# Kernel optimization log

Hardware: AMD Instinct MI355X
Metric: run time of the kernel (lower is better)

The kernel has to match this reference:

```python
import jax, jax.numpy as jnp
import numpy as np

N = 50000   # nodes
E = 800000  # edges (avg degree 16)
F = 16      # input node feature dim
H = 64      # hidden_channels
G = 128     # number of graphs
L = 3       # num_layers
OUT = 8     # output_channels


def _glorot(key, shape):
    fan = shape[-2] + shape[-1]
    return jax.random.normal(key, shape, dtype=jnp.float32) * jnp.sqrt(2.0 / fan)


def setup_inputs() -> dict:
    key = jax.random.key(0)
    ks = jax.random.split(key, 16)
    z = lambda *s: jnp.zeros(s, jnp.float32)
    return {
        "x": jax.random.normal(ks[0], (N, F), jnp.float32),
        "pos": jax.random.normal(ks[1], (N, 3), jnp.float32),
        "edge_index": jax.random.randint(ks[2], (2, E), 0, N),
        "batch": jnp.sort(jax.random.randint(ks[3], (N,), 0, G)),
        "node_W1": _glorot(ks[4], (F, H)), "node_b1": z(H),
        "node_W2": _glorot(ks[5], (H, H)), "node_b2": z(H),
        "local_W1": _glorot(ks[6], (L, 2 * H + 3, H)), "local_b1": z(L, H),
        "local_W2": _glorot(ks[7], (L, H, H)), "local_b2": z(L, H),
        "global_W1": _glorot(ks[8], (L, H, H)), "global_b1": z(L, H),
        "global_W2": _glorot(ks[9], (L, H, H)), "global_b2": z(L, H),
        "lin1_W": _glorot(ks[10], (H, H // 2)), "lin1_b": z(H // 2),
        "lin2_W": _glorot(ks[11], (H // 2, OUT)), "lin2_b": z(OUT),
    }


def reference(x, pos, edge_index, batch,
              node_W1, node_b1, node_W2, node_b2,
              local_W1, local_b1, local_W2, local_b2,
              global_W1, global_b1, global_W2, global_b2,
              lin1_W, lin1_b, lin2_W, lin2_b):
    n = x.shape[0]
    src, dst = edge_index[0], edge_index[1]  # x_j = x[src], x_i = x[dst]
    # node_lin: Linear -> ReLU -> Linear
    h = jnp.maximum(x @ node_W1 + node_b1, 0.0) @ node_W2 + node_b2
    for l in range(L):
        # message: cat([x_i, x_j, pos_j]) -> local_nn (Linear, ReLU, Linear)
        m = jnp.concatenate([h[dst], h[src], pos[src]], axis=-1)  # [E, 2H+3]
        m = jnp.maximum(m @ local_W1[l] + local_b1[l], 0.0) @ local_W2[l] + local_b2[l]
        # aggregate: scatter-add over destination nodes
        agg = jax.ops.segment_sum(m, dst, num_segments=n)
        # global_nn (Linear, ReLU, Linear), then outer ReLU from forward loop
        h = jnp.maximum(agg @ global_W1[l] + global_b1[l], 0.0) @ global_W2[l] + global_b2[l]
        h = jnp.maximum(h, 0.0)
    h = jnp.maximum(h @ lin1_W + lin1_b, 0.0)
    out = h @ lin2_W + lin2_b  # [N, OUT]
    # graph readout: scatter-add over batch ids
    return jax.ops.segment_sum(out, batch, num_segments=G)  # [G, OUT]
```

## Files before the change

### kernel.cpp

```cpp
#include <hip/hip_runtime.h>

#define N_NODES 50000
#define N_EDGES 800000
#define NGRAPH  128
#define XPITCH  72
#define NB      391
#define HEPB    4096
#define SEPB    8192
#define HBLKS   ((N_EDGES + HEPB - 1) / HEPB)
#define NGRP    3125
#define STRIDE  64
#define SENT    N_NODES

typedef short bf16x8 __attribute__((ext_vector_type(8)));
typedef float f32x4  __attribute__((ext_vector_type(4)));


__device__ __forceinline__ float atomAddF(float* p, float v) {
#if defined(__gfx950__) || defined(__AMDGCN__)
    return unsafeAtomicAdd(p, v);
#else
    return atomicAdd(p, v);
#endif
}

__device__ __forceinline__ unsigned short f2bf(float x) {
    unsigned u = __builtin_bit_cast(unsigned, x);
    u += 0x7fffu + ((u >> 16) & 1u);
    return (unsigned short)(u >> 16);
}
__device__ __forceinline__ float bf2f(unsigned short h) {
    return __builtin_bit_cast(float, (unsigned)h << 16);
}

__device__ __forceinline__ f32x4 mk4(float b) { f32x4 a = {b, b, b, b}; return a; }

template<int NKC, int KROW>
__device__ __forceinline__ f32x4 w_tile(const bf16x8* a,
                                        const unsigned short* __restrict__ Wm,
                                        int nt, int col, int quad, f32x4 acc) {
    const unsigned short* wp = Wm + (nt * 16 + col) * KROW + quad * 8;
#pragma unroll
    for (int c = 0; c < NKC; ++c) {
        bf16x8 b = *(const bf16x8*)(wp + c * 32);
        acc = __builtin_amdgcn_mfma_f32_16x16x32_bf16(a[c], b, acc, 0, 0, 0);
    }
    return acc;
}

template<int NKC>
__device__ __forceinline__ void a_load(const unsigned short* __restrict__ sl,
                                       int col, int quad, bf16x8* a) {
    a[0] = *(const bf16x8*)(sl + col * XPITCH + quad * 8);
    if (NKC > 1) a[1] = *(const bf16x8*)(sl + col * XPITCH + quad * 8 + 32);
}

__device__ __forceinline__ void w_store1(unsigned short* __restrict__ sl,
                                         int wv, int col, int quad, f32x4 acc,
                                         bool relu) {
#pragma unroll
    for (int r = 0; r < 4; ++r) {
        float x = acc[r];
        if (relu) x = fmaxf(x, 0.f);
        sl[(quad * 4 + r) * XPITCH + wv * 16 + col] = f2bf(x);
    }
}

__device__ __forceinline__ void g_store1(unsigned short* __restrict__ g, int gn0,
                                         int wv, int col, int quad, f32x4 acc) {
#pragma unroll
    for (int r = 0; r < 4; ++r) {
        int node = gn0 + quad * 4 + r;
        if (node < N_NODES)
            g[(size_t)node * 64 + wv * 16 + col] = f2bf(acc[r]);
    }
}

__device__ __forceinline__ void wave_agg4(const int* dg, unsigned short* __restrict__ sl,
                                          const unsigned short* __restrict__ u,
                                          const unsigned short* __restrict__ vin,
                                          const unsigned short* __restrict__ srcList,
                                          int gn0, int wv, int lane) {
    int sub = lane & 15, q = lane >> 4;
    int n0 = gn0 + wv * 4;
    ushort4 uu4[4];
#pragma unroll
    for (int mi = 0; mi < 4; ++mi)
        uu4[mi] = *(const ushort4*)(u + (size_t)(n0 + mi) * 64 + sub * 4);

#pragma unroll
    for (int mi = 0; mi < 4; ++mi) {
        int m = wv * 4 + mi;
        float u0 = bf2f(uu4[mi].x), u1 = bf2f(uu4[mi].y);
        float u2 = bf2f(uu4[mi].z), u3 = bf2f(uu4[mi].w);
        int pdeg = (dg[m] + 15) & ~15;
        size_t b = (size_t)(n0 + mi) * STRIDE;
        float a0 = 0.f, a1 = 0.f, a2 = 0.f, a3 = 0.f;

        for (int g0 = 0; g0 < pdeg; g0 += 16) {
            ushort4 ss = *(const ushort4*)(srcList + b + g0 + 4 * q);
            int s0 = ss.x, s1 = ss.y, s2 = ss.z, s3 = ss.w;
            ushort4 w0 = *(const ushort4*)(vin + (size_t)s0 * 64 + sub * 4);
            ushort4 w1 = *(const ushort4*)(vin + (size_t)s1 * 64 + sub * 4);
            ushort4 w2 = *(const ushort4*)(vin + (size_t)s2 * 64 + sub * 4);
            ushort4 w3 = *(const ushort4*)(vin + (size_t)s3 * 64 + sub * 4);
            a0 += fmaxf(u0 + bf2f(w0.x), 0.f) + fmaxf(u0 + bf2f(w1.x), 0.f)
                + fmaxf(u0 + bf2f(w2.x), 0.f) + fmaxf(u0 + bf2f(w3.x), 0.f);
            a1 += fmaxf(u1 + bf2f(w0.y), 0.f) + fmaxf(u1 + bf2f(w1.y), 0.f)
                + fmaxf(u1 + bf2f(w2.y), 0.f) + fmaxf(u1 + bf2f(w3.y), 0.f);
            a2 += fmaxf(u2 + bf2f(w0.z), 0.f) + fmaxf(u2 + bf2f(w1.z), 0.f)
                + fmaxf(u2 + bf2f(w2.z), 0.f) + fmaxf(u2 + bf2f(w3.z), 0.f);
            a3 += fmaxf(u3 + bf2f(w0.w), 0.f) + fmaxf(u3 + bf2f(w1.w), 0.f)
                + fmaxf(u3 + bf2f(w2.w), 0.f) + fmaxf(u3 + bf2f(w3.w), 0.f);
        }

        a0 += __shfl_xor(a0, 16); a0 += __shfl_xor(a0, 32);
        a1 += __shfl_xor(a1, 16); a1 += __shfl_xor(a1, 32);
        a2 += __shfl_xor(a2, 16); a2 += __shfl_xor(a2, 32);
        a3 += __shfl_xor(a3, 16); a3 += __shfl_xor(a3, 32);

        if (q == 0) {
            ushort4 o;
            o.x = f2bf(a0); o.y = f2bf(a1); o.z = f2bf(a2); o.w = f2bf(a3);
            *(ushort4*)&sl[m * XPITCH + sub * 4] = o;
        }
    }
}

#define OFF_NW1T  0
#define OFF_NW2T  2048
#define OFF_LYR   6144
#define LYR_SZ    20480
#define OFF_LIN1T 67584
#define OFF_LIN2T 69632
#define WT_TOTAL  70144

__global__ __launch_bounds__(256) void kPrep(
    const float* __restrict__ nW1, const float* __restrict__ lW1,
    const float* __restrict__ gW2,
    const float* __restrict__ lin1W, const float* __restrict__ lin2W,
    unsigned short* __restrict__ WT, int* __restrict__ gHist,
    int* __restrict__ doneCnt, float* __restrict__ out,
    unsigned short* __restrict__ v0, unsigned short* __restrict__ v1) {
    int i = blockIdx.x * 256 + threadIdx.x;
    if (blockIdx.x == 0) {
        for (int k = threadIdx.x; k < NB; k += 256) gHist[k] = 0;
        for (int k = threadIdx.x; k < NGRAPH * 8; k += 256) out[k] = 0.f;
        if (threadIdx.x == 0) *doneCnt = 0;
    }
    if (i < 64) {
        v0[(size_t)N_NODES * 64 + i] = 0xFF80;
        v1[(size_t)N_NODES * 64 + i] = 0xFF80;
    }
    if (i >= WT_TOTAL) return;
    int j = i;
    if (j < 2048) {
        int n = j >> 5, k = j & 31;
        WT[i] = (k < 16) ? f2bf(nW1[k * 64 + n]) : 0;
        return;
    }
    j -= 2048;
    if (j < 4096) return;
    j -= 4096;
    if (j < 3 * LYR_SZ) {
        int l = j / LYR_SZ;  j -= l * LYR_SZ;
        int m = j >> 12;     j &= 4095;
        if (m == 2 || m == 3 || (l == 0 && m < 2)) return;
        int n = j >> 6, k = j & 63;
        const float* src;
        if (m == 0)      src = lW1 + (size_t)l * 131 * 64;
        else if (m == 1) src = lW1 + (size_t)l * 131 * 64 + 64 * 64;
        else             src = gW2 + (size_t)l * 4096;
        WT[i] = f2bf(src[k * 64 + n]);
        return;
    }
    j -= 3 * LYR_SZ;
    if (j < 2048) {
        int n = j >> 6, k = j & 63;
        WT[i] = f2bf(lin1W[k * 32 + n]);
        return;
    }
    j -= 2048;
    {
        int n = j >> 5, k = j & 31;
        WT[i] = (n < 8) ? f2bf(lin2W[k * 8 + n]) : 0;
    }
}

__global__ __launch_bounds__(256) void kHist(
    const int* __restrict__ ei, int* __restrict__ gHist,
    int* __restrict__ bucketOff, int* __restrict__ cursor,
    int* __restrict__ doneCnt,
    const float* __restrict__ nW2, const float* __restrict__ lW1,
    const float* __restrict__ lW2, const float* __restrict__ gW1,
    const float* __restrict__ nb2, const float* __restrict__ lb1,
    const float* __restrict__ lb2,
    unsigned short* __restrict__ WT, float* __restrict__ fb) {
    __shared__ int h[NB];
    __shared__ int s0[512], s1[512];
    __shared__ int amLast;
    __shared__ float foldP[64 * 65];
    int tid = threadIdx.x;

    if (blockIdx.x >= HBLKS) {
        int f = blockIdx.x - HBLKS;
        const float* Wl;
        const float* Wr;
        size_t slot;
        if (f == 0)      { Wl = nW2;          Wr = lW1;            slot = OFF_LYR; }
        else if (f == 1) { Wl = nW2;          Wr = lW1 + 64 * 64;  slot = OFF_LYR + 4096; }
        else { int l = f - 2;
               Wl = lW2 + (size_t)l * 4096;   Wr = gW1 + (size_t)l * 4096;
               slot = OFF_LYR + (size_t)l * LYR_SZ + 2 * 4096; }

        int n = tid & 63;
        int w = tid >> 6;
        float acc[16];
#pragma unroll
        for (int i2 = 0; i2 < 16; ++i2) acc[i2] = 0.f;
        for (int t0 = 0; t0 < 64; t0 += 16) {
            float wr[16];
#pragma unroll
            for (int tt = 0; tt < 16; ++tt) wr[tt] = Wr[(t0 + tt) * 64 + n];
#pragma unroll
            for (int i2 = 0; i2 < 16; ++i2) {
                int kk = w * 16 + i2;
#pragma unroll
                for (int tt = 0; tt < 16; ++tt)
                    acc[i2] += Wl[kk * 64 + t0 + tt] * wr[tt];
            }
        }
#pragma unroll
        for (int i2 = 0; i2 < 16; ++i2)
            foldP[(w * 16 + i2) * 65 + n] = acc[i2];
        __syncthreads();
        for (int idx = tid; idx < 4096; idx += 256) {
            int nn = idx >> 6, kk = idx & 63;
            WT[slot + idx] = f2bf(foldP[kk * 65 + nn]);
        }
        if (tid < 64) {
            if (f == 0) {
                float s = 0.f;
                for (int t = 0; t < 64; ++t) s += nb2[t] * lW1[t * 64 + tid];
                fb[tid] = s;
            } else if (f == 1) {
                float s = 0.f;
                for (int t = 0; t < 64; ++t) s += nb2[t] * lW1[(64 + t) * 64 + tid];
                fb[64 + tid] = s + lb1[tid];
            } else {
                int l = f - 2;
                float s = 0.f;
                for (int t = 0; t < 64; ++t)
                    s += lb2[l * 64 + t] * gW1[(size_t)l * 4096 + t * 64 + tid];
                fb[128 + l * 64 + tid] = s;
            }
        }
        return;
    }

    for (int i = tid; i < NB; i += 256) h[i] = 0;
    __syncthreads();
    int base = blockIdx.x * HEPB;
#pragma unroll
    for (int k = 0; k < HEPB; k += 256) {
        int e = base + k + tid;
        if (e < N_EDGES) atomicAdd(&h[ei[N_EDGES + e] >> 7], 1);
    }
    __syncthreads();
    for (int i = tid; i < NB; i += 256)
        if (h[i]) atomicAdd(&gHist[i], h[i]);

    __threadfence();
    if (tid == 0) amLast = (atomicAdd(doneCnt, 1) == HBLKS - 1);
    __syncthreads();
    if (!amLast) return;
    __threadfence();

    for (int e = tid; e < 512; e += 256)
        s0[e] = (e < NB) ? atomicAdd(&gHist[e], 0) : 0;
    __syncthreads();
    int* sp = s0; int* dp = s1;
    for (int off = 1; off < 512; off <<= 1) {
        for (int e = tid; e < 512; e += 256)
            dp[e] = sp[e] + ((e >= off) ? sp[e - off] : 0);
        __syncthreads();
        int* t = sp; sp = dp; dp = t;
    }
    for (int e = tid; e < NB; e += 256) {
        int cnt = atomicAdd(&gHist[e], 0);
        int excl = sp[e] - cnt;
        bucketOff[e] = excl;
        cursor[e] = excl;
    }
    if (tid == 0) bucketOff[NB] = sp[NB - 1];
}

__global__ __launch_bounds__(256) void kScat(const int* __restrict__ ei,
                                             int* __restrict__ cursor,
                                             int* __restrict__ packs) {
    __shared__ int sdata[SEPB];
    __shared__ int hist[NB];
    __shared__ int loff[NB + 1];
    __shared__ int gbase[NB];
    __shared__ int sc0[512], sc1[512];
    int tid = threadIdx.x;
    int base = blockIdx.x * SEPB;
    int nE = min(SEPB, N_EDGES - base);

    for (int i = tid; i < NB; i += 256) hist[i] = 0;
    __syncthreads();

    int myPack[SEPB / 256];
    unsigned short myRank[SEPB / 256];
#pragma unroll
    for (int kk = 0; kk < SEPB / 256; ++kk) {
        int e = base + kk * 256 + tid;
        if (e < N_EDGES) {
            int s = ei[e], d = ei[N_EDGES + e];
            myPack[kk] = (s << 16) | d;
            myRank[kk] = (unsigned short)atomicAdd(&hist[d >> 7], 1);
        }
    }
    __syncthreads();

    for (int e = tid; e < 512; e += 256) sc0[e] = (e < NB) ? hist[e] : 0;
    __syncthreads();
    int* sp = sc0; int* dp = sc1;
    for (int off = 1; off < 512; off <<= 1) {
        for (int e = tid; e < 512; e += 256)
            dp[e] = sp[e] + ((e >= off) ? sp[e - off] : 0);
        __syncthreads();
        int* t = sp; sp = dp; dp = t;
    }
    for (int e = tid; e < NB; e += 256) loff[e] = sp[e] - hist[e];
    if (tid == 0) loff[NB] = sp[NB - 1];
    __syncthreads();

    for (int e = tid; e < NB; e += 256)
        gbase[e] = hist[e] ? atomicAdd(&cursor[e], hist[e]) : 0;
#pragma unroll
    for (int kk = 0; kk < SEPB / 256; ++kk) {
        int e = base + kk * 256 + tid;
        if (e < N_EDGES) {
            int p = myPack[kk];
            int b = (p & 0xffff) >> 7;
            sdata[loff[b] + myRank[kk]] = p;
        }
    }
    __syncthreads();

    for (int i = tid; i < nE; i += 256) {
        int p = sdata[i];
        int b = (p & 0xffff) >> 7;
        packs[gbase[b] + (i - loff[b])] = p;
    }
}

__global__ __launch_bounds__(256) void kSortA(
    const int* __restrict__ bucketOff, const int* __restrict__ packs,
    unsigned short* __restrict__ srcList, int* __restrict__ degArr,
    const float* __restrict__ x, const float* __restrict__ pos,
    const unsigned short* __restrict__ WT, const float* __restrict__ fb,
    const float* __restrict__ nb1,
    const float* __restrict__ lW1f,
    unsigned short* __restrict__ u, unsigned short* __restrict__ v) {
    __shared__ int cur[128];
    __shared__ unsigned short SL[2][16 * XPITCH];
    __shared__ float pw[48];

    int tid = threadIdx.x;
    if (blockIdx.x < NB) {
        int nbk = blockIdx.x;
        int nodeBase = nbk * 128;
        int nvalid = min(128, N_NODES - nodeBase);
        int eb = bucketOff[nbk], ee = bucketOff[nbk + 1];

        if (tid < 128) cur[tid] = 0;
        __syncthreads();
        for (int i = eb + tid; i < ee; i += 256) {
            int p = packs[i];
            int node = p & 127;
            int r = atomicAdd(&cur[node], 1);
            if (r < STRIDE)
                srcList[(size_t)(nodeBase + node) * STRIDE + r] =
                    (unsigned short)(((unsigned)p) >> 16);
        }
        __syncthreads();
        if (tid < nvalid) {
            int d = min(cur[tid], STRIDE);
            degArr[nodeBase + tid] = d;
            int pd = (d + 15) & ~15;
            size_t b2 = (size_t)(nodeBase + tid) * STRIDE;
            for (int r = d; r < pd; ++r) srcList[b2 + r] = (unsigned short)SENT;
        }
        return;
    }

    int gn0 = (blockIdx.x - NB) * 16;
    int lane = tid & 63;
    int wv = __builtin_amdgcn_readfirstlane(tid >> 6);
    int col = lane & 15, quad = lane >> 4;

    for (int idx = tid; idx < 512; idx += 256) {
        int m = idx >> 5, k = idx & 31;
        int node = gn0 + m;
        float val = (k < 16) ? x[(size_t)node * 16 + k] : 0.f;
        SL[0][m * XPITCH + k] = f2bf(val);
    }
    if (tid < 48) {
        int node = gn0 + tid / 3;
        pw[tid] = pos[(size_t)node * 3 + tid % 3];
    }
    __syncthreads();

    bf16x8 a[2];
    f32x4 acc;

    a_load<1>(SL[0], col, quad, a);
    acc = w_tile<1, 32>(a, WT + OFF_NW1T, wv, col, quad, mk4(nb1[wv * 16 + col]));
    w_store1(SL[1], wv, col, quad, acc, true);
    __syncthreads();

    const unsigned short* FA = WT + OFF_LYR;
    const unsigned short* FB = FA + 4096;
    const float* W1c = lW1f + 128 * 64;
    int ch = wv * 16 + col;

    a_load<2>(SL[1], col, quad, a);
    acc = w_tile<2, 64>(a, FA, wv, col, quad, mk4(fb[ch]));
    g_store1(u, gn0, wv, col, quad, acc);

    acc = w_tile<2, 64>(a, FB, wv, col, quad, mk4(fb[64 + ch]));
    float w0 = W1c[ch], w1 = W1c[64 + ch], w2 = W1c[128 + ch];
#pragma unroll
    for (int r = 0; r < 4; ++r) {
        int rr = quad * 4 + r;
        acc[r] += pw[rr * 3 + 0] * w0 + pw[rr * 3 + 1] * w1 + pw[rr * 3 + 2] * w2;
    }
    g_store1(v, gn0, wv, col, quad, acc);
}

__global__ __launch_bounds__(256) void kB(
    const float* __restrict__ pos, const int* __restrict__ degArr,
    const unsigned short* __restrict__ srcList,
    const unsigned short* __restrict__ WT, const float* __restrict__ fb, int l,
    const float* __restrict__ gb1, const float* __restrict__ gb2,
    const float* __restrict__ lW1f_next, const float* __restrict__ b1n,
    unsigned short* __restrict__ u,
    const unsigned short* __restrict__ vin,
    unsigned short* __restrict__ vout) {
    __shared__ unsigned short SL[2][16 * XPITCH];
    __shared__ float pw[48];
    __shared__ int dgW[16];
    int tid = threadIdx.x;
    int lane = tid & 63;
    int wv = __builtin_amdgcn_readfirstlane(tid >> 6);
    int gn0 = blockIdx.x * 16;
    int col = lane & 15, quad = lane >> 4;

    const unsigned short* LYR = WT + OFF_LYR + (size_t)l * LYR_SZ;
    const unsigned short* GT   = LYR + 2 * 4096;
    const unsigned short* gW2T = LYR + 4 * 4096;
    const unsigned short* aTn = WT + OFF_LYR + (size_t)(l + 1) * LYR_SZ;
    const unsigned short* bTn = aTn + 4096;
    const float* lbg = fb + 128 + l * 64;

    if (tid < 48) {
        int node = gn0 + tid / 3;
        pw[tid] = pos[(size_t)node * 3 + tid % 3];
    }
    if (tid < 16) dgW[tid] = degArr[gn0 + tid];
    __syncthreads();

    wave_agg4(dgW, SL[0], u, vin, srcList, gn0, wv, lane);
    __syncthreads();

    bf16x8 a[2];
    f32x4 acc;
    float dgr[4];
#pragma unroll
    for (int r = 0; r < 4; ++r) dgr[r] = (float)dgW[quad * 4 + r];

    int ch = wv * 16 + col;
    {
        float bb = lbg[ch];
        float g1 = gb1[ch];
        f32x4 init = {dgr[0] * bb + g1, dgr[1] * bb + g1,
                      dgr[2] * bb + g1, dgr[3] * bb + g1};
        a_load<2>(SL[0], col, quad, a);
        acc = w_tile<2, 64>(a, GT, wv, col, quad, init);
    }
    w_store1(SL[1], wv, col, quad, acc, true);
    __syncthreads();

    a_load<2>(SL[1], col, quad, a);
    acc = w_tile<2, 64>(a, gW2T, wv, col, quad, mk4(gb2[ch]));
    w_store1(SL[0], wv, col, quad, acc, true);
    __syncthreads();

    a_load<2>(SL[0], col, quad, a);
    acc = w_tile<2, 64>(a, aTn, wv, col, quad, mk4(0.f));
    g_store1(u, gn0, wv, col, quad, acc);

    const float* W1c = lW1f_next + 128 * 64;
    acc = w_tile<2, 64>(a, bTn, wv, col, quad, mk4(b1n[ch]));
    float w0 = W1c[ch], w1 = W1c[64 + ch], w2 = W1c[128 + ch];
#pragma unroll
    for (int r = 0; r < 4; ++r) {
        int rr = quad * 4 + r;
        acc[r] += pw[rr * 3 + 0] * w0 + pw[rr * 3 + 1] * w1 + pw[rr * 3 + 2] * w2;
    }
    g_store1(vout, gn0, wv, col, quad, acc);
}

__global__ __launch_bounds__(256) void kC(
    const int* __restrict__ degArr, const unsigned short* __restrict__ srcList,
    const int* __restrict__ batch, const unsigned short* __restrict__ WT,
    const float* __restrict__ fb,
    const float* __restrict__ gb1, const float* __restrict__ gb2,
    const float* __restrict__ lin1b, const float* __restrict__ lin2b,
    const unsigned short* __restrict__ u, const unsigned short* __restrict__ vin,
    float* __restrict__ out) {
    __shared__ unsigned short SL[2][16 * XPITCH];
    __shared__ int dgW[16];
    __shared__ int batchW[16];
    __shared__ float bins[16 * 8];
    int tid = threadIdx.x;
    int lane = tid & 63;
    int wv = __builtin_amdgcn_readfirstlane(tid >> 6);
    int gn0 = blockIdx.x * 16;
    int col = lane & 15, quad = lane >> 4;

    const unsigned short* LYR = WT + OFF_LYR + 2 * LYR_SZ;
    const unsigned short* GT   = LYR + 2 * 4096;
    const unsigned short* gW2T = LYR + 4 * 4096;
    const unsigned short* lin1T = WT + OFF_LIN1T;
    const unsigned short* lin2T = WT + OFF_LIN2T;
    const float* lbg = fb + 128 + 2 * 64;

    if (tid < 16) dgW[tid] = degArr[gn0 + tid];
    if (tid >= 32 && tid < 48) batchW[tid - 32] = batch[gn0 + tid - 32];
    if (tid >= 128 && tid < 256) bins[tid - 128] = 0.f;
    __syncthreads();

    wave_agg4(dgW, SL[0], u, vin, srcList, gn0, wv, lane);
    __syncthreads();

    bf16x8 a[2];
    f32x4 acc;
    float dgr[4];
#pragma unroll
    for (int r = 0; r < 4; ++r) dgr[r] = (float)dgW[quad * 4 + r];

    int ch = wv * 16 + col;
    {
        float bb = lbg[ch];
        float g1 = gb1[ch];
        f32x4 init = {dgr[0] * bb + g1, dgr[1] * bb + g1,
                      dgr[2] * bb + g1, dgr[3] * bb + g1};
        a_load<2>(SL[0], col, quad, a);
        acc = w_tile<2, 64>(a, GT, wv, col, quad, init);
    }
    w_store1(SL[1], wv, col, quad, acc, true);
    __syncthreads();

    a_load<2>(SL[1], col, quad, a);
    acc = w_tile<2, 64>(a, gW2T, wv, col, quad, mk4(gb2[ch]));
    w_store1(SL[0], wv, col, quad, acc, true);
    __syncthreads();

    a_load<2>(SL[0], col, quad, a);
    if (wv < 2) {
        acc = w_tile<2, 64>(a, lin1T, wv, col, quad, mk4(lin1b[wv * 16 + col]));
        w_store1(SL[1], wv, col, quad, acc, true);
    }
    __syncthreads();

    if (wv == 0) {
        a_load<1>(SL[1], col, quad, a);
        f32x4 o = w_tile<1, 32>(a, lin2T, 0, col, quad,
                                mk4(col < 8 ? lin2b[col] : 0.f));
        int gmin = batchW[0];
        if (col < 8) {
#pragma unroll
            for (int r = 0; r < 4; ++r) {
                int nl = quad * 4 + r;
                atomicAdd(&bins[(batchW[nl] - gmin) * 8 + col], o[r]);
            }
        }
    }
    __syncthreads();
    int gmin = batchW[0];
    int nb8 = (batchW[15] - gmin + 1) * 8;
    for (int idx = tid; idx < nb8; idx += 256)
        atomAddF(&out[gmin * 8 + idx], bins[idx]);
}

extern "C" void kernel_launch(void* const* d_in, const int* in_sizes, int n_in,
                              void* d_out, int out_size, void* d_ws, size_t ws_size,
                              hipStream_t stream) {
    const float* x     = (const float*)d_in[0];
    const float* pos   = (const float*)d_in[1];
    const int*   ei    = (const int*)d_in[2];
    const int*   batch = (const int*)d_in[3];
    const float* nW1   = (const float*)d_in[4];
    const float* nb1   = (const float*)d_in[5];
    const float* nW2   = (const float*)d_in[6];
    const float* nb2   = (const float*)d_in[7];
    const float* lW1   = (const float*)d_in[8];
    const float* lb1   = (const float*)d_in[9];
    const float* lW2   = (const float*)d_in[10];
    const float* lb2   = (const float*)d_in[11];
    const float* gW1   = (const float*)d_in[12];
    const float* gb1   = (const float*)d_in[13];
    const float* gW2   = (const float*)d_in[14];
    const float* gb2   = (const float*)d_in[15];
    const float* lin1W = (const float*)d_in[16];
    const float* lin1b = (const float*)d_in[17];
    const float* lin2W = (const float*)d_in[18];
    const float* lin2b = (const float*)d_in[19];
    float* out = (float*)d_out;

    unsigned short* u  = (unsigned short*)d_ws;
    unsigned short* v0 = u + (size_t)N_NODES * 64;
    unsigned short* v1 = v0 + (size_t)(N_NODES + 1) * 64;
    unsigned short* WT = v1 + (size_t)(N_NODES + 1) * 64;
    int* gHist = (int*)(WT + WT_TOTAL);
    int* bucketOff = gHist + NB;
    int* cursor = bucketOff + NB + 1;
    int* doneCnt = cursor + NB;
    int* degArr = doneCnt + 1;
    float* fbias = (float*)(degArr + N_NODES);
    int* packs = (int*)(fbias + 320);
    unsigned short* srcList = (unsigned short*)(packs + N_EDGES);

    kPrep<<<(WT_TOTAL + 255) / 256, 256, 0, stream>>>(nW1, lW1, gW2, lin1W, lin2W,
                                                      WT, gHist, doneCnt, out,
                                                      v0, v1);
    kHist<<<HBLKS + 5, 256, 0, stream>>>(ei, gHist, bucketOff, cursor, doneCnt,
                                         nW2, lW1, lW2, gW1, nb2, lb1, lb2,
                                         WT, fbias);
    kScat<<<(N_EDGES + SEPB - 1) / SEPB, 256, 0, stream>>>(ei, cursor, packs);
    kSortA<<<NB + NGRP, 256, 0, stream>>>(bucketOff, packs, srcList, degArr,
                                          x, pos, WT, fbias, nb1, lW1, u, v0);

    kB<<<NGRP, 256, 0, stream>>>(
        pos, degArr, srcList, WT, fbias, 0,
        gb1 + 0, gb2 + 0,
        lW1 + (size_t)1 * 131 * 64, lb1 + 64,
        u, v0, v1);
    kB<<<NGRP, 256, 0, stream>>>(
        pos, degArr, srcList, WT, fbias, 1,
        gb1 + 64, gb2 + 64,
        lW1 + (size_t)2 * 131 * 64, lb1 + 128,
        u, v1, v0);
    kC<<<NGRP, 256, 0, stream>>>(
        degArr, srcList, batch, WT, fbias,
        gb1 + 128, gb2 + 128, lin1b, lin2b,
        u, v0, out);
}
```

Baseline: 248.4 us.

## Fuse edge scatter with node-embedding blocks; split bucket sort into separate kernel

The edge scatter pass now runs in the same launch as the initial node MLP/projection blocks, and the per-node bucket sort moves into its own small kernel. The scatter drops the shared-memory local prefix sum and staging, writing packs straight to global memory at gbase plus rank, which gives uncoalesced writes. Edge order inside a bucket becomes nondeterministic, but the later per-node sort does not depend on that order. The aim is to overlap scatter work with the dense node work and cut synchronisation and shared-memory traffic.

After: 242.1 us. 2.6% less time.

```diff
diff --git a/kernel.cpp b/kernel.cpp
--- a/kernel.cpp
+++ b/kernel.cpp
@@ -8,6 +8,7 @@
 #define HEPB    4096
 #define SEPB    8192
 #define HBLKS   ((N_EDGES + HEPB - 1) / HEPB)
+#define SBLKS   ((N_EDGES + SEPB - 1) / SEPB)
 #define NGRP    3125
 #define STRIDE  64
 #define SENT    N_NODES
@@ -295,108 +296,55 @@
     if (tid == 0) bucketOff[NB] = sp[NB - 1];
 }
 
-__global__ __launch_bounds__(256) void kScat(const int* __restrict__ ei,
-                                             int* __restrict__ cursor,
-                                             int* __restrict__ packs) {
-    __shared__ int sdata[SEPB];
-    __shared__ int hist[NB];
-    __shared__ int loff[NB + 1];
-    __shared__ int gbase[NB];
-    __shared__ int sc0[512], sc1[512];
-    int tid = threadIdx.x;
-    int base = blockIdx.x * SEPB;
-    int nE = min(SEPB, N_EDGES - base);
-
-    for (int i = tid; i < NB; i += 256) hist[i] = 0;
-    __syncthreads();
-
-    int myPack[SEPB / 256];
-    unsigned short myRank[SEPB / 256];
-#pragma unroll
-    for (int kk = 0; kk < SEPB / 256; ++kk) {
-        int e = base + kk * 256 + tid;
-        if (e < N_EDGES) {
-            int s = ei[e], d = ei[N_EDGES + e];
-            myPack[kk] = (s << 16) | d;
-            myRank[kk] = (unsigned short)atomicAdd(&hist[d >> 7], 1);
-        }
-    }
-    __syncthreads();
-
-    for (int e = tid; e < 512; e += 256) sc0[e] = (e < NB) ? hist[e] : 0;
-    __syncthreads();
-    int* sp = sc0; int* dp = sc1;
-    for (int off = 1; off < 512; off <<= 1) {
-        for (int e = tid; e < 512; e += 256)
-            dp[e] = sp[e] + ((e >= off) ? sp[e - off] : 0);
-        __syncthreads();
-        int* t = sp; sp = dp; dp = t;
-    }
-    for (int e = tid; e < NB; e += 256) loff[e] = sp[e] - hist[e];
-    if (tid == 0) loff[NB] = sp[NB - 1];
-    __syncthreads();
-
-    for (int e = tid; e < NB; e += 256)
-        gbase[e] = hist[e] ? atomicAdd(&cursor[e], hist[e]) : 0;
-#pragma unroll
-    for (int kk = 0; kk < SEPB / 256; ++kk) {
-        int e = base + kk * 256 + tid;
-        if (e < N_EDGES) {
-            int p = myPack[kk];
-            int b = (p & 0xffff) >> 7;
-            sdata[loff[b] + myRank[kk]] = p;
-        }
-    }
-    __syncthreads();
-
-    for (int i = tid; i < nE; i += 256) {
-        int p = sdata[i];
-        int b = (p & 0xffff) >> 7;
-        packs[gbase[b] + (i - loff[b])] = p;
-    }
-}
-
-__global__ __launch_bounds__(256) void kSortA(
-    const int* __restrict__ bucketOff, const int* __restrict__ packs,
-    unsigned short* __restrict__ srcList, int* __restrict__ degArr,
+__global__ __launch_bounds__(256) void kScatA(
+    const int* __restrict__ ei, int* __restrict__ cursor,
+    int* __restrict__ packs,
     const float* __restrict__ x, const float* __restrict__ pos,
     const unsigned short* __restrict__ WT, const float* __restrict__ fb,
     const float* __restrict__ nb1,
     const float* __restrict__ lW1f,
     unsigned short* __restrict__ u, unsigned short* __restrict__ v) {
-    __shared__ int cur[128];
+    __shared__ int hist[NB];
+    __shared__ int gbase[NB];
     __shared__ unsigned short SL[2][16 * XPITCH];
     __shared__ float pw[48];
-
     int tid = threadIdx.x;
-    if (blockIdx.x < NB) {
-        int nbk = blockIdx.x;
-        int nodeBase = nbk * 128;
-        int nvalid = min(128, N_NODES - nodeBase);
-        int eb = bucketOff[nbk], ee = bucketOff[nbk + 1];
-
-        if (tid < 128) cur[tid] = 0;
+
+    if (blockIdx.x < SBLKS) {
+        int base = blockIdx.x * SEPB;
+        for (int i = tid; i < NB; i += 256) hist[i] = 0;
         __syncthreads();
-        for (int i = eb + tid; i < ee; i += 256) {
-            int p = packs[i];
-            int node = p & 127;
-            int r = atomicAdd(&cur[node], 1);
-            if (r < STRIDE)
-                srcList[(size_t)(nodeBase + node) * STRIDE + r] =
-                    (unsigned short)(((unsigned)p) >> 16);
+
+        int myPack[SEPB / 256];
+        unsigned short myRank[SEPB / 256];
+#pragma unroll
+        for (int kk = 0; kk < SEPB / 256; ++kk) {
+            int e = base + kk * 256 + tid;
+            if (e < N_EDGES) {
+                int s = ei[e], d = ei[N_EDGES + e];
+                myPack[kk] = (s << 16) | d;
+                myRank[kk] = (unsigned short)atomicAdd(&hist[d >> 7], 1);
+            }
         }
         __syncthreads();
-        if (tid < nvalid) {
-            int d = min(cur[tid], STRIDE);
-            degArr[nodeBase + tid] = d;
-            int pd = (d + 15) & ~15;
-            size_t b2 = (size_t)(nodeBase + tid) * STRIDE;
-            for (int r = d; r < pd; ++r) srcList[b2 + r] = (unsigned short)SENT;
+
+        for (int b = tid; b < NB; b += 256)
+            gbase[b] = hist[b] ? atomicAdd(&cursor[b], hist[b]) : 0;
+        __syncthreads();
+
+#pragma unroll
+        for (int kk = 0; kk < SEPB / 256; ++kk) {
+            int e = base + kk * 256 + tid;
+            if (e < N_EDGES) {
+                int p = myPack[kk];
+                int b = (p & 0xffff) >> 7;
+                packs[gbase[b] + myRank[kk]] = p;
+            }
         }
         return;
     }
 
-    int gn0 = (blockIdx.x - NB) * 16;
+    int gn0 = (blockIdx.x - SBLKS) * 16;
     int lane = tid & 63;
     int wv = __builtin_amdgcn_readfirstlane(tid >> 6);
     int col = lane & 15, quad = lane >> 4;
@@ -438,6 +386,36 @@
         acc[r] += pw[rr * 3 + 0] * w0 + pw[rr * 3 + 1] * w1 + pw[rr * 3 + 2] * w2;
     }
     g_store1(v, gn0, wv, col, quad, acc);
+}
+
+__global__ __launch_bounds__(256) void kSort(
+    const int* __restrict__ bucketOff, const int* __restrict__ packs,
+    unsigned short* __restrict__ srcList, int* __restrict__ degArr) {
+    __shared__ int cur[128];
+    int tid = threadIdx.x;
+    int nbk = blockIdx.x;
+    int nodeBase = nbk * 128;
+    int nvalid = min(128, N_NODES - nodeBase);
+    int eb = bucketOff[nbk], ee = bucketOff[nbk + 1];
+
+    if (tid < 128) cur[tid] = 0;
+    __syncthreads();
+    for (int i = eb + tid; i < ee; i += 256) {
+        int p = packs[i];
+        int node = p & 127;
+        int r = atomicAdd(&cur[node], 1);
+        if (r < STRIDE)
+            srcList[(size_t)(nodeBase + node) * STRIDE + r] =
+                (unsigned short)(((unsigned)p) >> 16);
+    }
+    __syncthreads();
+    if (tid < nvalid) {
+        int d = min(cur[tid], STRIDE);
+        degArr[nodeBase + tid] = d;
+        int pd = (d + 15) & ~15;
+        size_t b2 = (size_t)(nodeBase + tid) * STRIDE;
+        for (int r = d; r < pd; ++r) srcList[b2 + r] = (unsigned short)SENT;
+    }
 }
 
 __global__ __launch_bounds__(256) void kB(
@@ -640,9 +618,9 @@
     kHist<<<HBLKS + 5, 256, 0, stream>>>(ei, gHist, bucketOff, cursor, doneCnt,
                                          nW2, lW1, lW2, gW1, nb2, lb1, lb2,
                                          WT, fbias);
-    kScat<<<(N_EDGES + SEPB - 1) / SEPB, 256, 0, stream>>>(ei, cursor, packs);
-    kSortA<<<NB + NGRP, 256, 0, stream>>>(bucketOff, packs, srcList, degArr,
-                                          x, pos, WT, fbias, nb1, lW1, u, v0);
+    kScatA<<<SBLKS + NGRP, 256, 0, stream>>>(ei, cursor, packs,
+                                             x, pos, WT, fbias, nb1, lW1, u, v0);
+    kSort<<<NB, 256, 0, stream>>>(bucketOff, packs, srcList, degArr);
 
     kB<<<NGRP, 256, 0, stream>>>(
         pos, degArr, srcList, WT, fbias, 0,
```
